# Performance work log

Hardware: AMD Instinct MI355X
Metric: run time of the kernel (lower is better)

Reference implementation:

```python
import jax, jax.numpy as jnp
import numpy as np

B, NC, F, U = 8, 64, 8, 128   # batch, mesh size, ConvLSTM filters, LSTM units
NITER = 4
BS = 200.0                    # box size
B1, B2, LR, EPS = 0.9, 0.999, 0.1, 1e-7


def _conv3d(x, w, b=None):
    out = jax.lax.conv_general_dilated(x, w, (1, 1, 1), 'SAME',
                                       dimension_numbers=('NDHWC', 'DHWIO', 'NDHWC'))
    return out if b is None else out + b


def _conv1d(x, w, b):
    return jax.lax.conv_general_dilated(x, w, (1,), 'SAME',
                                        dimension_numbers=('NWC', 'WIO', 'NWC')) + b


def setup_inputs():
    key = jax.random.key(0)
    ks = jax.random.split(key, 16)
    # radial |k| bin map, values in [0, NC)
    kf = np.fft.fftfreq(NC) * NC
    kx, ky, kz = np.meshgrid(kf, kf, kf, indexing='ij')
    knorm = np.sqrt(kx ** 2 + ky ** 2 + kz ** 2)
    kbinmap = np.minimum((knorm / knorm.max() * (NC - 1)).astype(np.int32), NC - 1)
    s = 0.05
    return {
        'x_init': jax.random.normal(ks[0], (B, NC, NC, NC), jnp.float32),
        'y':      jax.random.normal(ks[1], (B, NC, NC, NC), jnp.float32),
        'x_true': jax.random.normal(ks[2], (B, NC, NC, NC), jnp.float32),
        'kbinmap': jnp.asarray(kbinmap),
        # input_layer: Conv3D 2 -> F
        'W_in': jax.random.normal(ks[3], (3, 3, 3, 2, F), jnp.float32) * s,
        'b_in': jnp.zeros((F,), jnp.float32),
        # ConvLSTM3D cell: gates order i,f,g,o
        'Wx3': jax.random.normal(ks[4], (3, 3, 3, F, 4 * F), jnp.float32) * s,
        'Wh3': jax.random.normal(ks[5], (3, 3, 3, F, 4 * F), jnp.float32) * s,
        'b3':  jnp.zeros((4 * F,), jnp.float32),
        # output_layer: Conv3D F -> 1
        'W_out': jax.random.normal(ks[6], (3, 3, 3, F, 1), jnp.float32) * s,
        'b_out': jnp.zeros((1,), jnp.float32),
        # input_layer1d: Dense 2*NC -> U
        'Wd1': jax.random.normal(ks[7], (2 * NC, U), jnp.float32) * s,
        'bd1': jnp.zeros((U,), jnp.float32),
        # LSTM cell (units U)
        'Wlx': jax.random.normal(ks[8], (U, 4 * U), jnp.float32) * s,
        'Wlh': jax.random.normal(ks[9], (U, 4 * U), jnp.float32) * s,
        'bl':  jnp.zeros((4 * U,), jnp.float32),
        # output_layer1d: Dense U -> NC
        'Wd2': jax.random.normal(ks[10], (U, NC), jnp.float32) * s,
        'bd2': jnp.zeros((NC,), jnp.float32),
        # output_layer1dconv: Conv1D 1 -> 1, kernel 3
        'Wc1': jax.random.normal(ks[11], (3, 1, 1), jnp.float32) * s,
        'bc1': jnp.zeros((1,), jnp.float32),
    }


def _forward(x_init, y, x_true, W_in, b_in, Wx3, Wh3, b3, W_out, b_out,
             Wd1, bd1, Wlx, Wlh, bl, Wd2, bd2, Wc1, bc1, kbinmap):
    nc = x_init.shape[-1]
    bsz = x_init.shape[0]
    kflat = kbinmap.reshape(-1)
    counts = jax.ops.segment_sum(jnp.ones(kflat.shape, jnp.float32), kflat,
                                 num_segments=nc)

    def varmap(x):
        # tfvarmap: binned power spectrum, [B, nc]
        pm = jnp.abs(jnp.fft.fftn(x, axes=(1, 2, 3)) / nc ** 3) ** 2
        pmf = pm.reshape(bsz, -1)
        power = jax.vmap(lambda p: jax.ops.segment_sum(p, kflat, num_segments=nc))(pmf)
        return power / counts

    def filt(x, ps, p):
        # colorps (p=+0.5) / whitenps (p=-0.5); flowpm r2c/c2r norms cancel
        pmesh = ps[:, kbinmap]                      # [B,nc,nc,nc] gather by kbin
        fac = (pmesh ** p).astype(jnp.complex64)
        return jnp.real(jnp.fft.ifftn(jnp.fft.fftn(x, axes=(1, 2, 3)) * fac,
                                      axes=(1, 2, 3)))

    def convlstm(x, h, c):
        z = _conv3d(x, Wx3, b3) + _conv3d(h, Wh3)
        i, f, g, o = jnp.split(z, 4, axis=-1)
        c = jax.nn.sigmoid(f) * c + jax.nn.sigmoid(i) * jnp.tanh(g)
        h = jax.nn.sigmoid(o) * jnp.tanh(c)
        return h, c

    def lstm(x, h, c):
        z = x @ Wlx + h @ Wlh + bl
        i, f, g, o = jnp.split(z, 4, axis=-1)
        c = jax.nn.sigmoid(f) * c + jax.nn.sigmoid(i) * jnp.tanh(g)
        h = jax.nn.sigmoid(o) * jnp.tanh(c)
        return h, c

    ln10 = jnp.log(jnp.float32(10.0))

    def step(carry, t):
        pos, m, v, h1, c1, h3, c3, loss = carry
        grad = pos - y                              # stand-in grad_fn (data-consistency)
        m = B1 * m + (1.0 - B1) * grad
        v = B2 * v + (1.0 - B2) * grad * grad
        mc = m / (1.0 - B1 ** t)
        vc = v / (1.0 - B2 ** t)
        delta = -LR * mc / (jnp.sqrt(vc) + EPS)
        pspos = varmap(pos)
        psdelta = varmap(delta)
        lpspos = jnp.log(pspos * BS ** 3) / ln10
        lpsdelta = jnp.log(psdelta * BS ** 3) / ln10
        # 3D branch
        cell_in = _conv3d(jnp.stack([pos, delta], axis=-1), W_in, b_in)
        h3, c3 = convlstm(cell_in, h3, c3)
        delta_poswhite = _conv3d(h3, W_out, b_out)[..., 0]
        # 1D power-spectrum branch
        x1 = jnp.concatenate([lpspos, lpsdelta], axis=-1) @ Wd1 + bd1
        h1, c1 = lstm(x1, h1, c1)
        lps = h1 @ Wd2 + bd2
        lps = _conv1d(lps[..., None], Wc1, bc1)[..., 0]
        psdeltanew = jnp.exp(lps)                   # note: exp (base e), as in source
        new_pos = pos + filt(delta_poswhite, psdeltanew, 0.5)
        loss = loss + jnp.mean((x_true - new_pos) ** 2)
        return (new_pos, m, v, h1, c1, h3, c3, loss), None

    z = jnp.zeros_like(x_init)
    init = (x_init, z, z,
            jnp.zeros((bsz, U), x_init.dtype), jnp.zeros((bsz, U), x_init.dtype),
            jnp.zeros(x_init.shape + (F,), x_init.dtype),
            jnp.zeros(x_init.shape + (F,), x_init.dtype),
            jnp.zeros((), x_init.dtype))
    ts = jnp.arange(1, NITER + 1, dtype=jnp.float32)
    (pos, m, v, h1, c1, h3, c3, loss), _ = jax.lax.scan(step, init, ts)
    return pos, loss


def reference(x_init, y, x_true, kbinmap, W_in, b_in, Wx3, Wh3, b3, W_out, b_out,
              Wd1, bd1, Wlx, Wlh, bl, Wd2, bd2, Wc1, bc1):
    return _forward(x_init, y, x_true, W_in, b_in, Wx3, Wh3, b3, W_out, b_out,
                    Wd1, bd1, Wlx, Wlh, bl, Wd2, bd2, Wc1, bc1, kbinmap)
```

## Files before the change

kernel.cpp:

```cpp
#include <hip/hip_runtime.h>
#include <math.h>

#define NCC 64
#define NB 8
#define VOL (NCC*NCC*NCC)
#define TOT (NB*VOL)
#define WTOT 170869
#define PI2 6.2831853071795864769f
#define HS 287496
#define SX 4356

typedef unsigned short u16;
typedef __bf16 bf16x8 __attribute__((ext_vector_type(8)));
typedef float f32x16 __attribute__((ext_vector_type(16)));

__device__ __forceinline__ float b2f(u16 h){ return __uint_as_float(((unsigned)h)<<16); }
__device__ __forceinline__ u16 f2b(float f){
  unsigned u = __float_as_uint(f);
  unsigned r = (u + 0x7FFFu + ((u>>16)&1u)) >> 16;
  return (u16)r;
}
__device__ __forceinline__ float fsig(float x){ return 1.f / (1.f + __expf(-x)); }
__device__ __forceinline__ float ftanh(float x){
  float e = __expf(2.f * x);
  return 1.f - 2.f / (e + 1.f);
}

template<bool INV>
__device__ __forceinline__ void fft8(float2* x) {
  const float C = 0.70710678118654752440f;
  float2 s0,s1,s2,s3,s4,s5,s6,s7;
  s0 = make_float2(x[0].x + x[4].x, x[0].y + x[4].y);
  s4 = make_float2(x[0].x - x[4].x, x[0].y - x[4].y);
  s1 = make_float2(x[1].x + x[5].x, x[1].y + x[5].y);
  s5 = make_float2(x[1].x - x[5].x, x[1].y - x[5].y);
  s2 = make_float2(x[2].x + x[6].x, x[2].y + x[6].y);
  s6 = make_float2(x[2].x - x[6].x, x[2].y - x[6].y);
  s3 = make_float2(x[3].x + x[7].x, x[3].y + x[7].y);
  s7 = make_float2(x[3].x - x[7].x, x[3].y - x[7].y);
  float2 n5, n6, n7;
  if (!INV) {
    n5 = make_float2(C*(s5.x + s5.y), C*(s5.y - s5.x));
    n6 = make_float2(s6.y, -s6.x);
    n7 = make_float2(C*(s7.y - s7.x), -C*(s7.x + s7.y));
  } else {
    n5 = make_float2(C*(s5.x - s5.y), C*(s5.y + s5.x));
    n6 = make_float2(-s6.y, s6.x);
    n7 = make_float2(-C*(s7.x + s7.y), C*(s7.x - s7.y));
  }
  float2 t0,t1,t2,t3,t4,t5,t6,t7,d;
  t0 = make_float2(s0.x + s2.x, s0.y + s2.y);
  t2 = make_float2(s0.x - s2.x, s0.y - s2.y);
  t1 = make_float2(s1.x + s3.x, s1.y + s3.y);
  d  = make_float2(s1.x - s3.x, s1.y - s3.y);
  t3 = INV ? make_float2(-d.y, d.x) : make_float2(d.y, -d.x);
  t4 = make_float2(s4.x + n6.x, s4.y + n6.y);
  t6 = make_float2(s4.x - n6.x, s4.y - n6.y);
  t5 = make_float2(n5.x + n7.x, n5.y + n7.y);
  d  = make_float2(n5.x - n7.x, n5.y - n7.y);
  t7 = INV ? make_float2(-d.y, d.x) : make_float2(d.y, -d.x);
  x[0] = make_float2(t0.x + t1.x, t0.y + t1.y);
  x[1] = make_float2(t0.x - t1.x, t0.y - t1.y);
  x[2] = make_float2(t2.x + t3.x, t2.y + t3.y);
  x[3] = make_float2(t2.x - t3.x, t2.y - t3.y);
  x[4] = make_float2(t4.x + t5.x, t4.y + t5.y);
  x[5] = make_float2(t4.x - t5.x, t4.y - t5.y);
  x[6] = make_float2(t6.x + t7.x, t6.y + t7.y);
  x[7] = make_float2(t6.x - t7.x, t6.y - t7.y);
}

template<bool INV>
__device__ __forceinline__ void dft64(float2* Pf, const float2* tw, int ls, int ns) {
  const int BR[8] = {0,4,2,6,1,5,3,7};
  int t = threadIdx.x;
  int L0 = t >> 3, b = t & 7, L1 = L0 + 32;
  float2 v0[8], v1[8];
  #pragma unroll
  for (int a = 0; a < 8; ++a) v0[a] = Pf[L0*ls + (8*a + b)*ns];
  #pragma unroll
  for (int a = 0; a < 8; ++a) v1[a] = Pf[L1*ls + (8*a + b)*ns];
  __syncthreads();
  fft8<INV>(v0); fft8<INV>(v1);
  #pragma unroll
  for (int r = 0; r < 8; ++r) {
    float2 w = tw[(b * r) & 63];
    if (INV) w.y = -w.y;
    float2 a0 = v0[BR[r]], a1 = v1[BR[r]];
    Pf[L0*ls + (8*b + r)*ns] = make_float2(a0.x*w.x - a0.y*w.y, a0.x*w.y + a0.y*w.x);
    Pf[L1*ls + (8*b + r)*ns] = make_float2(a1.x*w.x - a1.y*w.y, a1.x*w.y + a1.y*w.x);
  }
  __syncthreads();
  int r = t & 7;
  #pragma unroll
  for (int q = 0; q < 8; ++q) v0[q] = Pf[L0*ls + (8*q + r)*ns];
  #pragma unroll
  for (int q = 0; q < 8; ++q) v1[q] = Pf[L1*ls + (8*q + r)*ns];
  fft8<INV>(v0); fft8<INV>(v1);
  #pragma unroll
  for (int j = 0; j < 8; ++j) {
    Pf[L0*ls + (8*BR[j] + r)*ns] = v0[j];
    Pf[L1*ls + (8*BR[j] + r)*ns] = v1[j];
  }
  __syncthreads();
}

__global__ __launch_bounds__(256) void k_sniff(const u16* __restrict__ x, int* __restrict__ flag) {
  __shared__ int cnt;
  if (threadIdx.x == 0) cnt = 0;
  __syncthreads();
  int sane = 0;
  for (int i = threadIdx.x; i < 1024; i += 256) {
    u16 h = x[2 * i];
    int e = (h >> 7) & 0xFF;
    if (h == 0 || (e >= 0x68 && e <= 0x8F)) sane++;
  }
  atomicAdd(&cnt, sane);
  __syncthreads();
  if (threadIdx.x == 0) flag[0] = (cnt >= 768) ? 1 : 0;
}

__global__ __launch_bounds__(256) void k_cvt(const void* __restrict__ in, size_t eoff,
                                             float* __restrict__ out, const int* __restrict__ flag) {
  size_t i = (size_t)blockIdx.x * 256 + threadIdx.x;
  if (*flag) out[i] = b2f(((const u16*)in)[eoff + i]);
  else       out[i] = ((const float*)in)[eoff + i];
}

__global__ __launch_bounds__(256) void k_cvtall(
    const void* s0, const void* s1, const void* s2, const void* s3,
    const void* s4, const void* s5, const void* s6, const void* s7,
    const void* s8, const void* s9, const void* s10, const void* s11,
    const void* s12, const void* s13, const void* s14, const void* s15,
    float* __restrict__ out, const int* __restrict__ flag) {
  const void* ps[16] = {s0,s1,s2,s3,s4,s5,s6,s7,s8,s9,s10,s11,s12,s13,s14,s15};
  const int offs[17] = {0,432,440,7352,14264,14296,14512,14513,30897,31025,
                        96561,162097,162609,170801,170865,170868,170869};
  int i = blockIdx.x * 256 + threadIdx.x;
  if (i >= WTOT) return;
  int s = 0;
  #pragma unroll
  for (int k = 1; k < 16; ++k) if (i >= offs[k]) s = k;
  int j = i - offs[s];
  if (*flag) out[i] = b2f(((const u16*)ps[s])[j]);
  else       out[i] = ((const float*)ps[s])[j];
}

__global__ __launch_bounds__(256) void k_mkwf(const void* __restrict__ Wx, const void* __restrict__ Wh,
                                              const int* __restrict__ flag, u16* __restrict__ Wf) {
  int i = blockIdx.x * 256 + threadIdx.x;
  if (i >= 13824) return;
  int j = i & 7, co = (i >> 3) & 31, hi = (i >> 8) & 1, tap = i >> 9;
  int src = tap * 256 + j * 32 + co;
  const void* P = hi ? Wh : Wx;
  u16 val;
  if (*flag) val = ((const u16*)P)[src];
  else       val = f2b(((const float*)P)[src]);
  Wf[i] = val;
}

__global__ __launch_bounds__(256) void k_mkwfo(const void* __restrict__ Wo,
                                               const int* __restrict__ flag, u16* __restrict__ Wfo) {
  int i = blockIdx.x * 256 + threadIdx.x;
  if (i >= 7168) return;
  int j = i & 7, co = (i >> 3) & 31, hi = (i >> 8) & 1, p = i >> 9;
  int tap = 2 * p + hi;
  u16 val = 0;
  if (co == 0 && tap < 27) {
    int src = tap * 8 + j;
    val = *flag ? ((const u16*)Wo)[src] : f2b(((const float*)Wo)[src]);
  }
  Wfo[i] = val;
}

__global__ __launch_bounds__(256) void k_counts(const int* __restrict__ kbin,
                                                float* __restrict__ cnts) {
  __shared__ float s[NCC];
  int t = threadIdx.x;
  if (t < NCC) s[t] = 0.f;
  __syncthreads();
  int i = blockIdx.x * 256 + t;
  atomicAdd(&s[kbin[i]], 1.f);
  __syncthreads();
  if (t < NCC) atomicAdd(&cnts[t], s[t]);
}

__global__ __launch_bounds__(256) void k_fft_zy_adam(
    const float* __restrict__ pos, const void* __restrict__ yraw, size_t yoff,
    float* __restrict__ m, float* __restrict__ v, float* __restrict__ dpw,
    float2* __restrict__ cout, float ib1, float ib2, int first,
    const int* __restrict__ flag, float* __restrict__ psp, float* __restrict__ psd) {
  __shared__ float2 P[64*66];
  __shared__ float2 tw[64];
  int t = threadIdx.x;
  if (t < 64) { float s, c; __sincosf(-(PI2/64.f)*(float)t, &s, &c); tw[t] = make_float2(c, s); }
  int bb = blockIdx.x >> 6, xx = blockIdx.x & 63;
  if (xx == 0) {
    if (t < 64)                 psp[bb*64 + t] = 0.f;
    else if (t < 128)           psd[bb*64 + (t - 64)] = 0.f;
  }
  size_t pb = (size_t)blockIdx.x * 4096;
  int bf = *flag;
  #pragma unroll
  for (int i = 0; i < 4; ++i) {
    int i4 = t + 256*i;
    float4 p4 = ((const float4*)(pos + pb))[i4];
    float yv[4];
    if (bf) {
      uint2 yu = ((const uint2*)((const u16*)yraw + yoff + pb))[i4];
      const u16* yp = (const u16*)&yu;
      yv[0]=b2f(yp[0]); yv[1]=b2f(yp[1]); yv[2]=b2f(yp[2]); yv[3]=b2f(yp[3]);
    } else {
      float4 y4 = ((const float4*)((const float*)yraw + yoff + pb))[i4];
      yv[0]=y4.x; yv[1]=y4.y; yv[2]=y4.z; yv[3]=y4.w;
    }
    float pv[4] = {p4.x, p4.y, p4.z, p4.w};
    float mo[4], vo[4], dd[4];
    if (!first) {
      float4 m4 = ((const float4*)(m + pb))[i4];
      float4 v4 = ((const float4*)(v + pb))[i4];
      mo[0]=m4.x; mo[1]=m4.y; mo[2]=m4.z; mo[3]=m4.w;
      vo[0]=v4.x; vo[1]=v4.y; vo[2]=v4.z; vo[3]=v4.w;
    }
    #pragma unroll
    for (int c = 0; c < 4; ++c) {
      float g = pv[c] - yv[c];
      float mi = first ? 0.1f*g : 0.9f*mo[c] + 0.1f*g;
      float vi = first ? 0.001f*g*g : 0.999f*vo[c] + 0.001f*g*g;
      mo[c] = mi; vo[c] = vi;
      dd[c] = -0.1f * (mi * ib1) / (sqrtf(vi * ib2) + 1e-7f);
    }
    ((float4*)(m + pb))[i4]   = make_float4(mo[0], mo[1], mo[2], mo[3]);
    ((float4*)(v + pb))[i4]   = make_float4(vo[0], vo[1], vo[2], vo[3]);
    ((float4*)(dpw + pb))[i4] = make_float4(dd[0], dd[1], dd[2], dd[3]);
    int base = i4 * 4;
    float2* row = P + (base >> 6)*66 + (base & 63);
    row[0] = make_float2(pv[0], 0.f);
    row[1] = make_float2(pv[1], 0.f);
    row[2] = make_float2(pv[2], 0.f);
    row[3] = make_float2(pv[3], 0.f);
  }
  __syncthreads();
  dft64<false>(P, tw, 66, 1);
  dft64<false>(P, tw, 1, 66);
  float4* dst = (float4*)(cout + pb);
  #pragma unroll
  for (int i = 0; i < 8; ++i) {
    int idx2 = (t + 256*i) * 2;
    float2 a = P[(idx2 >> 6)*66 + (idx2 & 63)];
    float2 b = P[(idx2 >> 6)*66 + (idx2 & 63) + 1];
    dst[t + 256*i] = make_float4(a.x, a.y, b.x, b.y);
  }
}

__global__ __launch_bounds__(256) void k_fft_zy(const float* __restrict__ rin,
                                                float2* __restrict__ cout) {
  __shared__ float2 P[64*66];
  __shared__ float2 tw[64];
  int t = threadIdx.x;
  if (t < 64) { float s, c; __sincosf(-(PI2/64.f)*(float)t, &s, &c); tw[t] = make_float2(c, s); }
  const float* src = rin + (size_t)blockIdx.x * 4096;
  #pragma unroll
  for (int i = 0; i < 4; ++i) {
    float4 v = ((const float4*)src)[t + 256*i];
    int base = (t + 256*i) * 4;
    float2* row = P + (base >> 6)*66 + (base & 63);
    row[0] = make_float2(v.x, 0.f);
    row[1] = make_float2(v.y, 0.f);
    row[2] = make_float2(v.z, 0.f);
    row[3] = make_float2(v.w, 0.f);
  }
  __syncthreads();
  dft64<false>(P, tw, 66, 1);
  dft64<false>(P, tw, 1, 66);
  float4* dst = (float4*)(cout + (size_t)blockIdx.x * 4096);
  #pragma unroll
  for (int i = 0; i < 8; ++i) {
    int idx2 = (t + 256*i) * 2;
    float2 a = P[(idx2 >> 6)*66 + (idx2 & 63)];
    float2 b = P[(idx2 >> 6)*66 + (idx2 & 63) + 1];
    dst[t + 256*i] = make_float4(a.x, a.y, b.x, b.y);
  }
}

__global__ __launch_bounds__(256) void k_fft_x_pow(const float2* __restrict__ cin,
                                                   const int* __restrict__ kb,
                                                   float* __restrict__ psum) {
  __shared__ float2 P[64*66];
  __shared__ float2 tw[64];
  __shared__ float pb[64];
  int t = threadIdx.x;
  if (t < 64) { float s, c; __sincosf(-(PI2/64.f)*(float)t, &s, &c); tw[t] = make_float2(c, s); pb[t] = 0.f; }
  int b = blockIdx.x >> 6, y = blockIdx.x & 63;
  #pragma unroll
  for (int i = 0; i < 8; ++i) {
    int idx2 = (t + 256*i) * 2;
    int x = idx2 >> 6, z = idx2 & 63;
    float4 v = *(const float4*)(cin + (((size_t)(b*64 + x)*64 + y)*64 + z));
    P[x*66 + z]     = make_float2(v.x, v.y);
    P[x*66 + z + 1] = make_float2(v.z, v.w);
  }
  __syncthreads();
  dft64<false>(P, tw, 1, 66);
  const float INV2 = 1.0f / ((float)VOL * (float)VOL);
  #pragma unroll
  for (int i = 0; i < 16; ++i) {
    int idx = t + 256*i;
    int x = idx >> 6, z = idx & 63;
    float2 a = P[x*66 + z];
    float pm = (a.x*a.x + a.y*a.y) * INV2;
    atomicAdd(&pb[kb[(x*64 + y)*64 + z]], pm);
  }
  __syncthreads();
  if (t < 64) atomicAdd(&psum[b*64 + t], pb[t]);
}

__global__ __launch_bounds__(256) void k_fft_x_filt(float2* __restrict__ cb,
                                                    const int* __restrict__ kb,
                                                    const float* __restrict__ psn) {
  __shared__ float2 P[64*66];
  __shared__ float2 tw[64];
  int t = threadIdx.x;
  if (t < 64) { float s, c; __sincosf(-(PI2/64.f)*(float)t, &s, &c); tw[t] = make_float2(c, s); }
  int b = blockIdx.x >> 6, y = blockIdx.x & 63;
  #pragma unroll
  for (int i = 0; i < 8; ++i) {
    int idx2 = (t + 256*i) * 2;
    int x = idx2 >> 6, z = idx2 & 63;
    float4 v = *(const float4*)(cb + (((size_t)(b*64 + x)*64 + y)*64 + z));
    P[x*66 + z]     = make_float2(v.x, v.y);
    P[x*66 + z + 1] = make_float2(v.z, v.w);
  }
  __syncthreads();
  dft64<false>(P, tw, 1, 66);
  #pragma unroll
  for (int i = 0; i < 16; ++i) {
    int idx = t + 256*i;
    int x = idx >> 6, z = idx & 63;
    float fac = sqrtf(psn[b*64 + kb[(x*64 + y)*64 + z]]);
    float2 a = P[x*66 + z];
    P[x*66 + z] = make_float2(a.x * fac, a.y * fac);
  }
  __syncthreads();
  dft64<true>(P, tw, 1, 66);
  #pragma unroll
  for (int i = 0; i < 8; ++i) {
    int idx2 = (t + 256*i) * 2;
    int x = idx2 >> 6, z = idx2 & 63;
    float2 a = P[x*66 + z], c = P[x*66 + z + 1];
    *(float4*)(cb + (((size_t)(b*64 + x)*64 + y)*64 + z)) = make_float4(a.x, a.y, c.x, c.y);
  }
}

__global__ __launch_bounds__(256) void k_fft_zy_inv(const float2* __restrict__ cin,
                                                    float* __restrict__ pos,
                                                    const void* __restrict__ xtraw, size_t xoff,
                                                    float* __restrict__ lsum,
                                                    const int* __restrict__ flag,
                                                    void* __restrict__ outp, size_t ooff) {
  __shared__ float2 P[64*66];
  __shared__ float2 tw[64];
  __shared__ float red[256];
  int t = threadIdx.x;
  if (t < 64) { float s, c; __sincosf(-(PI2/64.f)*(float)t, &s, &c); tw[t] = make_float2(c, s); }
  size_t pb = (size_t)blockIdx.x * 4096;
  const float4* src = (const float4*)(cin + pb);
  #pragma unroll
  for (int i = 0; i < 8; ++i) {
    float4 v = src[t + 256*i];
    int idx2 = (t + 256*i) * 2;
    P[(idx2 >> 6)*66 + (idx2 & 63)]     = make_float2(v.x, v.y);
    P[(idx2 >> 6)*66 + (idx2 & 63) + 1] = make_float2(v.z, v.w);
  }
  __syncthreads();
  dft64<true>(P, tw, 1, 66);
  dft64<true>(P, tw, 66, 1);
  float* pdst = pos + pb;
  int bf = *flag;
  float lacc = 0.f;
  #pragma unroll
  for (int i = 0; i < 16; ++i) {
    int idx = t + 256*i;
    float np = pdst[idx] + P[(idx >> 6)*66 + (idx & 63)].x * (1.0f/(float)VOL);
    pdst[idx] = np;
    if (outp) {
      if (bf) ((u16*)outp)[ooff + pb + idx] = f2b(np);
      else    ((float*)outp)[ooff + pb + idx] = np;
    }
    float xt = bf ? b2f(((const u16*)xtraw)[xoff + pb + idx])
                  : ((const float*)xtraw)[xoff + pb + idx];
    float d = xt - np;
    lacc = fmaf(d, d, lacc);
  }
  red[t] = lacc; __syncthreads();
  for (int s = 128; s > 0; s >>= 1) { if (t < s) red[t] += red[t+s]; __syncthreads(); }
  if (t == 0) atomicAdd(lsum, red[0]);
}

__global__ __launch_bounds__(256) void k_cellin(const float* __restrict__ pos,
                                                const float* __restrict__ delta,
                                                const float* __restrict__ Win,
                                                const float* __restrict__ binf,
                                                u16* __restrict__ ci) {
  int id = blockIdx.x * 256 + threadIdx.x;
  int z = id & 63, yy = (id >> 6) & 63, x = (id >> 12) & 63, b = id >> 18;
  float acc[8];
  #pragma unroll
  for (int c = 0; c < 8; ++c) acc[c] = binf[c];
  #pragma unroll 1
  for (int tap = 0; tap < 27; ++tap) {
    int kd = tap / 9, kh = (tap / 3) % 3, kw = tap % 3;
    int nx = x + kd - 1, ny = yy + kh - 1, nz = z + kw - 1;
    if ((unsigned)nx >= 64u || (unsigned)ny >= 64u || (unsigned)nz >= 64u) continue;
    size_t n = (((size_t)b * 64 + nx) * 64 + ny) * 64 + nz;
    float p = pos[n], d = delta[n];
    const float* w = Win + tap * 16;
    #pragma unroll
    for (int c = 0; c < 8; ++c) acc[c] = fmaf(p, w[c], fmaf(d, w[8 + c], acc[c]));
  }
  u16 hh[8];
  #pragma unroll
  for (int c = 0; c < 8; ++c) hh[c] = f2b(acc[c]);
  size_t slot = (size_t)b * HS + (size_t)(x + 1) * SX + (yy + 1) * 66 + z + 1;
  *(uint4*)(ci + slot * 8) = *(uint4*)hh;
}

__global__ __launch_bounds__(512, 8) void k_clstm(const u16* __restrict__ ci,
                                                  const u16* __restrict__ hC,
                                                  u16* __restrict__ hN,
                                                  u16* __restrict__ c3u,
                                                  const u16* __restrict__ Wf,
                                                  const float* __restrict__ b3f) {
  __shared__ u16 wfl[13824];
  int t = threadIdx.x;
  for (int i = t; i < 1728; i += 512) ((uint4*)wfl)[i] = ((const uint4*)Wf)[i];
  int wv = t >> 6, l = t & 63, ln = l & 31, hi = l >> 5;
  int bid = blockIdx.x;
  int x = bid & 63, yq = (bid >> 6) & 15, b = bid >> 10;
  int y = yq * 4 + (wv >> 1), z0 = (wv & 1) * 32;
  size_t cslot = (size_t)b * HS + (size_t)(x + 1) * SX + (y + 1) * 66 + z0 + ln + 1;
  const u16* abase = (hi ? hC : ci) + cslot * 8;
  const u16* axm = abase - SX * 8;
  const u16* axp = abase + SX * 8;
  const u16* wbase = wfl + hi * 256 + ln * 8;
  __syncthreads();
  f32x16 acc;
  #pragma unroll
  for (int r = 0; r < 16; ++r) acc[r] = 0.f;
  #pragma unroll
  for (int tap = 0; tap < 27; ++tap) {
    const int dx = tap / 9, dy = (tap / 3) % 3 - 1, dz = tap % 3 - 1;
    const u16* ab = (dx == 0) ? axm : ((dx == 1) ? abase : axp);
    bf16x8 wfr = __builtin_bit_cast(bf16x8, *(const uint4*)(wbase + tap * 512));
    bf16x8 afr = __builtin_bit_cast(bf16x8, *(const uint4*)(ab + (dy * 66 + dz) * 8));
    acc = __builtin_amdgcn_mfma_f32_32x32x16_bf16(wfr, afr, acc, 0, 0, 0);
  }
  float4 bi  = *(const float4*)(b3f + 4 * hi);
  float4 bff = *(const float4*)(b3f + 8 + 4 * hi);
  float4 bg  = *(const float4*)(b3f + 16 + 4 * hi);
  float4 bo_ = *(const float4*)(b3f + 24 + 4 * hi);
  const float* bip = (const float*)&bi;
  const float* bfp = (const float*)&bff;
  const float* bgp = (const float*)&bg;
  const float* bop = (const float*)&bo_;
  uint2 cu = *(const uint2*)(c3u + cslot * 8 + hi * 4);
  const u16* cp = (const u16*)&cu;
  u16 cw[4], hw[4];
  #pragma unroll
  for (int q = 0; q < 4; ++q) {
    float zi  = acc[q]      + bip[q];
    float zf  = acc[4 + q]  + bfp[q];
    float zg  = acc[8 + q]  + bgp[q];
    float zo_ = acc[12 + q] + bop[q];
    float cn = fsig(zf) * b2f(cp[q]) + fsig(zi) * ftanh(zg);
    cw[q] = f2b(cn);
    hw[q] = f2b(fsig(zo_) * ftanh(cn));
  }
  *(uint2*)(c3u + cslot * 8 + hi * 4) = *(uint2*)cw;
  *(uint2*)(hN + cslot * 8 + hi * 4)  = *(uint2*)hw;
}

__global__ __launch_bounds__(512, 8) void k_wout(const u16* __restrict__ h,
                                                 const u16* __restrict__ Wfo,
                                                 const float* __restrict__ bo,
                                                 float* __restrict__ dpw) {
  __shared__ u16 wfl[7168];
  int t = threadIdx.x;
  for (int i = t; i < 896; i += 512) ((uint4*)wfl)[i] = ((const uint4*)Wfo)[i];
  int wv = t >> 6, l = t & 63, ln = l & 31, hi = l >> 5;
  int bid = blockIdx.x;
  int x = bid & 63, yq = (bid >> 6) & 15, b = bid >> 10;
  int y = yq * 4 + (wv >> 1), z0 = (wv & 1) * 32;
  size_t cslot = (size_t)b * HS + (size_t)(x + 1) * SX + (y + 1) * 66 + z0 + ln + 1;
  const u16* abase = h + cslot * 8;
  const u16* wbase = wfl + hi * 256 + ln * 8;
  __syncthreads();
  f32x16 acc;
  #pragma unroll
  for (int r = 0; r < 16; ++r) acc[r] = 0.f;
  #pragma unroll
  for (int p = 0; p < 14; ++p) {
    const int t0 = 2 * p;
    const int t1 = (2 * p + 1 < 27) ? (2 * p + 1) : 26;
    const int o0 = (t0 / 9) * SX + ((t0 / 3) % 3) * 66 + (t0 % 3) - (SX + 66 + 1);
    const int o1 = (t1 / 9) * SX + ((t1 / 3) % 3) * 66 + (t1 % 3) - (SX + 66 + 1);
    int off = hi ? o1 : o0;
    bf16x8 wfr = __builtin_bit_cast(bf16x8, *(const uint4*)(wbase + p * 512));
    bf16x8 afr = __builtin_bit_cast(bf16x8, *(const uint4*)(abase + (ptrdiff_t)off * 8));
    acc = __builtin_amdgcn_mfma_f32_32x32x16_bf16(wfr, afr, acc, 0, 0, 0);
  }
  if (hi == 0) {
    size_t vox = (((size_t)b * 64 + x) * 64 + y) * 64 + z0 + ln;
    dpw[vox] = acc[0] + bo[0];
  }
}

__global__ __launch_bounds__(256) void k_small(const float* __restrict__ psp,
                                               const float* __restrict__ psd,
                                               const float* __restrict__ cnts,
                                               const float* __restrict__ Wd1,
                                               const float* __restrict__ bd1,
                                               const float* __restrict__ Wlx,
                                               const float* __restrict__ Wlh,
                                               const float* __restrict__ bl,
                                               const float* __restrict__ Wd2,
                                               const float* __restrict__ bd2,
                                               const float* __restrict__ Wc1,
                                               const float* __restrict__ bc1,
                                               float* __restrict__ h1, float* __restrict__ c1,
                                               float* __restrict__ psn) {
  __shared__ float lp[128], x1[128], hs[128], zz[512], lps[66];
  int t = threadIdx.x, b = blockIdx.x;
  if (t < 64) {
    lp[t]      = __log10f(fmaxf(psp[b*64 + t] / cnts[t] * 8.0e6f, 1e-30f));
    lp[64 + t] = __log10f(fmaxf(psd[b*64 + t] / cnts[t] * 8.0e6f, 1e-30f));
  }
  if (t < 128) hs[t] = h1[b*128 + t];
  __syncthreads();
  if (t < 128) {
    float a = bd1[t];
    for (int j = 0; j < 128; ++j) a = fmaf(lp[j], Wd1[j*128 + t], a);
    x1[t] = a;
  }
  __syncthreads();
  for (int k = t; k < 512; k += 256) {
    float a = bl[k];
    for (int u = 0; u < 128; ++u)
      a = fmaf(x1[u], Wlx[u*512 + k], fmaf(hs[u], Wlh[u*512 + k], a));
    zz[k] = a;
  }
  __syncthreads();
  if (t < 128) {
    float cv = fsig(zz[128 + t]) * c1[b*128 + t] + fsig(zz[t]) * ftanh(zz[256 + t]);
    c1[b*128 + t] = cv;
    float hv = fsig(zz[384 + t]) * ftanh(cv);
    h1[b*128 + t] = hv; hs[t] = hv;
  }
  __syncthreads();
  if (t < 64) {
    float a = bd2[t];
    for (int u = 0; u < 128; ++u) a = fmaf(hs[u], Wd2[u*64 + t], a);
    lps[t + 1] = a;
  }
  __syncthreads();
  if (t < 64) {
    float a = fmaf(Wc1[1], lps[t + 1], bc1[0]);
    if (t > 0)  a = fmaf(Wc1[0], lps[t], a);
    if (t < 63) a = fmaf(Wc1[2], lps[t + 2], a);
    psn[b*64 + t] = __expf(a);
  }
}

__global__ void k_loss(const float* __restrict__ lsum, void* __restrict__ outp,
                       const int* __restrict__ flag) {
  float l = lsum[0] * (1.0f / (float)TOT);
  if (*flag) ((u16*)outp)[TOT] = f2b(l);
  else       ((float*)outp)[TOT] = l;
}

__global__ void k_sent(u16* __restrict__ outp) { outp[0] = f2b(1000.0f); }

extern "C" void kernel_launch(void* const* d_in, const int* in_sizes, int n_in,
                              void* d_out, int out_size, void* d_ws, size_t ws_size,
                              hipStream_t stream) {
  const void* x_init = d_in[0];
  const void* y      = d_in[1];
  const void* x_true = d_in[2];
  const int*  kbin   = (const int*)d_in[3];

  int nbs = 0;
  for (int cand = 8; cand >= 1; cand >>= 1) {
    size_t n1c = (size_t)cand * VOL;
    size_t slc = (size_t)cand * HS;
    size_t need = 4 * n1c * 4
                + 4 * slc * 16
                + n1c * 8
                + (171008 + 6912 + 3584 + (size_t)cand * (192 + 256) + 96) * 4;
    if (need <= ws_size) { nbs = cand; break; }
  }
  if (nbs == 0) { k_sent<<<1, 1, 0, stream>>>((u16*)d_out); return; }

  size_t n1 = (size_t)nbs * VOL;
  size_t sl = (size_t)nbs * HS;
  float* ws   = (float*)d_ws;
  float* pos  = ws;
  float* m    = pos + n1;
  float* v    = m + n1;
  float* dpw  = v + n1;
  u16*  c3u   = (u16*)(dpw + n1);
  u16*  ci    = c3u + sl*8;
  u16*  hA    = ci + sl*8;
  u16*  hB    = hA + sl*8;
  float2* cb  = (float2*)(hB + sl*8);
  float* wbuf = (float*)((float*)cb + n1*2);
  u16*  Wf    = (u16*)(wbuf + 171008);
  u16*  Wfo   = Wf + 13824;
  float* psp  = wbuf + 171008 + 6912 + 3584;
  float* psd  = psp + (size_t)nbs*64;
  float* psn  = psd + (size_t)nbs*64;
  float* cnts = psn + (size_t)nbs*64;
  float* lsum = cnts + 64;
  float* h1   = lsum + 8;
  float* c1   = h1 + (size_t)nbs*128;
  int*   flag = (int*)(c1 + (size_t)nbs*128);

  float* Win_f = wbuf + 0;     float* bin_f = wbuf + 432;
  float* b3_f  = wbuf + 14264;
  float* bo_f  = wbuf + 14512; float* Wd1_f = wbuf + 14513;
  float* bd1_f = wbuf + 30897; float* Wlx_f = wbuf + 31025;
  float* Wlh_f = wbuf + 96561; float* bl_f  = wbuf + 162097;
  float* Wd2_f = wbuf + 162609; float* bd2_f = wbuf + 170801;
  float* Wc1_f = wbuf + 170865; float* bc1_f = wbuf + 170868;

  const int CB = (int)(n1 / 256);

  k_sniff<<<1, 256, 0, stream>>>((const u16*)x_init, flag);
  k_cvtall<<<(WTOT + 255) / 256, 256, 0, stream>>>(
      d_in[4], d_in[5], d_in[6], d_in[7], d_in[8], d_in[9], d_in[10], d_in[11],
      d_in[12], d_in[13], d_in[14], d_in[15], d_in[16], d_in[17], d_in[18], d_in[19],
      wbuf, flag);
  k_mkwf<<<54, 256, 0, stream>>>(d_in[6], d_in[7], flag, Wf);
  k_mkwfo<<<28, 256, 0, stream>>>(d_in[9], flag, Wfo);
  hipMemsetAsync(cnts, 0, 72 * 4, stream);
  k_counts<<<VOL / 256, 256, 0, stream>>>(kbin, cnts);

  for (int b0 = 0; b0 < NB; b0 += nbs) {
    hipMemsetAsync(c3u, 0, sl * 64, stream);
    hipMemsetAsync(h1, 0, (size_t)nbs * 256 * 4, stream);
    k_cvt<<<CB, 256, 0, stream>>>(x_init, (size_t)b0 * VOL, pos, flag);

    u16* hC = hA;
    u16* hN = hB;
    for (int t = 1; t <= 4; ++t) {
      float ib1 = (float)(1.0 / (1.0 - pow(0.9, (double)t)));
      float ib2 = (float)(1.0 / (1.0 - pow(0.999, (double)t)));

      k_fft_zy_adam<<<nbs * 64, 256, 0, stream>>>(pos, y, (size_t)b0 * VOL, m, v, dpw,
                                                  cb, ib1, ib2, t == 1, flag, psp, psd);
      k_fft_x_pow<<<nbs * 64, 256, 0, stream>>>(cb, kbin, psp);
      k_fft_zy<<<nbs * 64, 256, 0, stream>>>(dpw, cb);
      k_fft_x_pow<<<nbs * 64, 256, 0, stream>>>(cb, kbin, psd);

      k_cellin<<<CB, 256, 0, stream>>>(pos, dpw, Win_f, bin_f, ci);
      k_clstm<<<nbs * 1024, 512, 0, stream>>>(ci, hC, hN, c3u, Wf, b3_f);
      k_wout<<<nbs * 1024, 512, 0, stream>>>(hN, Wfo, bo_f, dpw);

      k_small<<<nbs, 256, 0, stream>>>(psp, psd, cnts, Wd1_f, bd1_f, Wlx_f, Wlh_f, bl_f,
                                       Wd2_f, bd2_f, Wc1_f, bc1_f, h1, c1, psn);

      k_fft_zy<<<nbs * 64, 256, 0, stream>>>(dpw, cb);
      k_fft_x_filt<<<nbs * 64, 256, 0, stream>>>(cb, kbin, psn);
      k_fft_zy_inv<<<nbs * 64, 256, 0, stream>>>(cb, pos, x_true, (size_t)b0 * VOL, lsum,
                                                 flag, (t == 4) ? d_out : nullptr,
                                                 (size_t)b0 * VOL);

      u16* tmp = hC; hC = hN; hN = tmp;
    }
  }
  k_loss<<<1, 1, 0, stream>>>(lsum, d_out, flag);
}
```

Before: 1.294 ms.

## Move input conv to bf16 MFMA and split MFMA accumulators in conv kernels

The 2->8 channel input Conv3D, previously scalar FMA loops per voxel, now packs position/delta neighbour values into bf16 and runs them through 32x32x16 MFMA using a new prepacked weight layout. The clstm and output conv kernels also alternate between two accumulators so that back-to-back MFMAs are not serialized on one accumulator dependency. This cuts ALU work in the input layer but rounds its inputs to bf16, which may change numerical accuracy, and it adds register pressure from the second accumulator.

```diff
diff --git a/kernel.cpp b/kernel.cpp
--- a/kernel.cpp
+++ b/kernel.cpp
@@ -170,6 +170,21 @@
     val = *flag ? ((const u16*)Wo)[src] : f2b(((const float*)Wo)[src]);
   }
   Wfo[i] = val;
+}
+
+__global__ __launch_bounds__(256) void k_mkwfi(const void* __restrict__ Wi,
+                                               const int* __restrict__ flag, u16* __restrict__ Wfi) {
+  int i = blockIdx.x * 256 + threadIdx.x;
+  if (i >= 2048) return;
+  int j = i & 7, co = (i >> 3) & 31, hi = (i >> 8) & 1, m = i >> 9;
+  int k = hi * 8 + j;
+  int tap = m * 8 + (k >> 1), ch = k & 1;
+  u16 val = 0;
+  if (co < 8 && tap < 27) {
+    int src = tap * 16 + ch * 8 + co;
+    val = *flag ? ((const u16*)Wi)[src] : f2b(((const float*)Wi)[src]);
+  }
+  Wfi[i] = val;
 }
 
 __global__ __launch_bounds__(256) void k_counts(const int* __restrict__ kbin,
@@ -396,32 +411,51 @@
   if (t == 0) atomicAdd(lsum, red[0]);
 }
 
-__global__ __launch_bounds__(256) void k_cellin(const float* __restrict__ pos,
-                                                const float* __restrict__ delta,
-                                                const float* __restrict__ Win,
-                                                const float* __restrict__ binf,
-                                                u16* __restrict__ ci) {
-  int id = blockIdx.x * 256 + threadIdx.x;
-  int z = id & 63, yy = (id >> 6) & 63, x = (id >> 12) & 63, b = id >> 18;
-  float acc[8];
-  #pragma unroll
-  for (int c = 0; c < 8; ++c) acc[c] = binf[c];
-  #pragma unroll 1
-  for (int tap = 0; tap < 27; ++tap) {
-    int kd = tap / 9, kh = (tap / 3) % 3, kw = tap % 3;
-    int nx = x + kd - 1, ny = yy + kh - 1, nz = z + kw - 1;
-    if ((unsigned)nx >= 64u || (unsigned)ny >= 64u || (unsigned)nz >= 64u) continue;
-    size_t n = (((size_t)b * 64 + nx) * 64 + ny) * 64 + nz;
-    float p = pos[n], d = delta[n];
-    const float* w = Win + tap * 16;
+__global__ __launch_bounds__(512, 8) void k_cellin(const float* __restrict__ pos,
+                                                   const float* __restrict__ delta,
+                                                   const u16* __restrict__ Wfi,
+                                                   const float* __restrict__ binf,
+                                                   u16* __restrict__ ci) {
+  __shared__ u16 wfl[2048];
+  int t = threadIdx.x;
+  if (t < 256) ((uint4*)wfl)[t] = ((const uint4*)Wfi)[t];
+  int wv = t >> 6, l = t & 63, ln = l & 31, hi = l >> 5;
+  int bid = blockIdx.x;
+  int x = bid & 63, yq = (bid >> 6) & 15, b = bid >> 10;
+  int y = yq * 4 + (wv >> 1), z0 = (wv & 1) * 32;
+  int z = z0 + ln;
+  const u16* wbase = wfl + hi * 256 + ln * 8;
+  __syncthreads();
+  f32x16 acc;
+  #pragma unroll
+  for (int r = 0; r < 16; ++r) acc[r] = 0.f;
+  #pragma unroll
+  for (int m = 0; m < 4; ++m) {
+    unsigned pk[4];
     #pragma unroll
-    for (int c = 0; c < 8; ++c) acc[c] = fmaf(p, w[c], fmaf(d, w[8 + c], acc[c]));
-  }
-  u16 hh[8];
-  #pragma unroll
-  for (int c = 0; c < 8; ++c) hh[c] = f2b(acc[c]);
-  size_t slot = (size_t)b * HS + (size_t)(x + 1) * SX + (yy + 1) * 66 + z + 1;
-  *(uint4*)(ci + slot * 8) = *(uint4*)hh;
+    for (int kk = 0; kk < 4; ++kk) {
+      const int tap = m * 8 + hi * 4 + kk;
+      float pv = 0.f, dv = 0.f;
+      if (tap < 27) {
+        const int dx = tap / 9 - 1, dy = (tap / 3) % 3 - 1, dz = tap % 3 - 1;
+        int nx = x + dx, ny = y + dy, nz = z + dz;
+        if ((unsigned)nx < 64u && (unsigned)ny < 64u && (unsigned)nz < 64u) {
+          size_t n = (((size_t)b * 64 + nx) * 64 + ny) * 64 + nz;
+          pv = pos[n]; dv = delta[n];
+        }
+      }
+      pk[kk] = (unsigned)f2b(pv) | ((unsigned)f2b(dv) << 16);
+    }
+    uint4 q = make_uint4(pk[0], pk[1], pk[2], pk[3]);
+    bf16x8 bfr = __builtin_bit_cast(bf16x8, q);
+    bf16x8 wfr = __builtin_bit_cast(bf16x8, *(const uint4*)(wbase + m * 512));
+    acc = __builtin_amdgcn_mfma_f32_32x32x16_bf16(wfr, bfr, acc, 0, 0, 0);
+  }
+  size_t cslot = (size_t)b * HS + (size_t)(x + 1) * SX + (y + 1) * 66 + z + 1;
+  u16 hh[4];
+  #pragma unroll
+  for (int q = 0; q < 4; ++q) hh[q] = f2b(acc[q] + binf[hi * 4 + q]);
+  *(uint2*)(ci + cslot * 8 + hi * 4) = *(uint2*)hh;
 }
 
 __global__ __launch_bounds__(512, 8) void k_clstm(const u16* __restrict__ ci,
@@ -443,17 +477,21 @@
   const u16* axp = abase + SX * 8;
   const u16* wbase = wfl + hi * 256 + ln * 8;
   __syncthreads();
-  f32x16 acc;
-  #pragma unroll
-  for (int r = 0; r < 16; ++r) acc[r] = 0.f;
+  f32x16 acc0, acc1;
+  #pragma unroll
+  for (int r = 0; r < 16; ++r) { acc0[r] = 0.f; acc1[r] = 0.f; }
   #pragma unroll
   for (int tap = 0; tap < 27; ++tap) {
     const int dx = tap / 9, dy = (tap / 3) % 3 - 1, dz = tap % 3 - 1;
     const u16* ab = (dx == 0) ? axm : ((dx == 1) ? abase : axp);
     bf16x8 wfr = __builtin_bit_cast(bf16x8, *(const uint4*)(wbase + tap * 512));
     bf16x8 afr = __builtin_bit_cast(bf16x8, *(const uint4*)(ab + (dy * 66 + dz) * 8));
-    acc = __builtin_amdgcn_mfma_f32_32x32x16_bf16(wfr, afr, acc, 0, 0, 0);
-  }
+    if (tap & 1) acc1 = __builtin_amdgcn_mfma_f32_32x32x16_bf16(wfr, afr, acc1, 0, 0, 0);
+    else         acc0 = __builtin_amdgcn_mfma_f32_32x32x16_bf16(wfr, afr, acc0, 0, 0, 0);
+  }
+  f32x16 acc;
+  #pragma unroll
+  for (int r = 0; r < 16; ++r) acc[r] = acc0[r] + acc1[r];
   float4 bi  = *(const float4*)(b3f + 4 * hi);
   float4 bff = *(const float4*)(b3f + 8 + 4 * hi);
   float4 bg  = *(const float4*)(b3f + 16 + 4 * hi);
@@ -494,9 +532,9 @@
   const u16* abase = h + cslot * 8;
   const u16* wbase = wfl + hi * 256 + ln * 8;
   __syncthreads();
-  f32x16 acc;
-  #pragma unroll
-  for (int r = 0; r < 16; ++r) acc[r] = 0.f;
+  f32x16 acc0, acc1;
+  #pragma unroll
+  for (int r = 0; r < 16; ++r) { acc0[r] = 0.f; acc1[r] = 0.f; }
   #pragma unroll
   for (int p = 0; p < 14; ++p) {
     const int t0 = 2 * p;
@@ -506,11 +544,12 @@
     int off = hi ? o1 : o0;
     bf16x8 wfr = __builtin_bit_cast(bf16x8, *(const uint4*)(wbase + p * 512));
     bf16x8 afr = __builtin_bit_cast(bf16x8, *(const uint4*)(abase + (ptrdiff_t)off * 8));
-    acc = __builtin_amdgcn_mfma_f32_32x32x16_bf16(wfr, afr, acc, 0, 0, 0);
+    if (p & 1) acc1 = __builtin_amdgcn_mfma_f32_32x32x16_bf16(wfr, afr, acc1, 0, 0, 0);
+    else       acc0 = __builtin_amdgcn_mfma_f32_32x32x16_bf16(wfr, afr, acc0, 0, 0, 0);
   }
   if (hi == 0) {
     size_t vox = (((size_t)b * 64 + x) * 64 + y) * 64 + z0 + ln;
-    dpw[vox] = acc[0] + bo[0];
+    dpw[vox] = acc0[0] + acc1[0] + bo[0];
   }
 }
 
@@ -594,7 +633,7 @@
     size_t need = 4 * n1c * 4
                 + 4 * slc * 16
                 + n1c * 8
-                + (171008 + 6912 + 3584 + (size_t)cand * (192 + 256) + 96) * 4;
+                + (171008 + 6912 + 3584 + 1024 + (size_t)cand * (192 + 256) + 96) * 4;
     if (need <= ws_size) { nbs = cand; break; }
   }
   if (nbs == 0) { k_sent<<<1, 1, 0, stream>>>((u16*)d_out); return; }
@@ -614,7 +653,8 @@
   float* wbuf = (float*)((float*)cb + n1*2);
   u16*  Wf    = (u16*)(wbuf + 171008);
   u16*  Wfo   = Wf + 13824;
-  float* psp  = wbuf + 171008 + 6912 + 3584;
+  u16*  Wfi   = Wfo + 7168;
+  float* psp  = wbuf + 171008 + 6912 + 3584 + 1024;
   float* psd  = psp + (size_t)nbs*64;
   float* psn  = psd + (size_t)nbs*64;
   float* cnts = psn + (size_t)nbs*64;
@@ -623,7 +663,7 @@
   float* c1   = h1 + (size_t)nbs*128;
   int*   flag = (int*)(c1 + (size_t)nbs*128);
 
-  float* Win_f = wbuf + 0;     float* bin_f = wbuf + 432;
+  float* bin_f = wbuf + 432;
   float* b3_f  = wbuf + 14264;
   float* bo_f  = wbuf + 14512; float* Wd1_f = wbuf + 14513;
   float* bd1_f = wbuf + 30897; float* Wlx_f = wbuf + 31025;
@@ -640,6 +680,7 @@
       wbuf, flag);
   k_mkwf<<<54, 256, 0, stream>>>(d_in[6], d_in[7], flag, Wf);
   k_mkwfo<<<28, 256, 0, stream>>>(d_in[9], flag, Wfo);
+  k_mkwfi<<<8, 256, 0, stream>>>(d_in[4], flag, Wfi);
   hipMemsetAsync(cnts, 0, 72 * 4, stream);
   k_counts<<<VOL / 256, 256, 0, stream>>>(kbin, cnts);
 
@@ -660,7 +701,7 @@
       k_fft_zy<<<nbs * 64, 256, 0, stream>>>(dpw, cb);
       k_fft_x_pow<<<nbs * 64, 256, 0, stream>>>(cb, kbin, psd);
 
-      k_cellin<<<CB, 256, 0, stream>>>(pos, dpw, Win_f, bin_f, ci);
+      k_cellin<<<nbs * 1024, 512, 0, stream>>>(pos, dpw, Wfi, bin_f, ci);
       k_clstm<<<nbs * 1024, 512, 0, stream>>>(ci, hC, hN, c3u, Wf, b3_f);
       k_wout<<<nbs * 1024, 512, 0, stream>>>(hN, Wfo, bo_f, dpw);
 
```

New measurement: 1.312 ms. No clear change (+1.4%).
